# Optimization experiments

Measured on AMD Instinct MI355X. Metric: run time of the kernel, lower is better.

Reference implementation:

```python
import jax, jax.numpy as jnp
import numpy as np

B, C, H, W, NH = 4, 96, 256, 256, 4


def setup_inputs() -> dict:
    key = jax.random.key(0)
    ks = jax.random.split(key, 8)
    s = 0.05  # keep pre-activations well-scaled
    return {
        "x": jax.random.normal(ks[0], (B, C, H, W), jnp.float32),
        "ff": jax.random.normal(ks[1], (B, C, H, W), jnp.float32),
        "w_q": jax.random.normal(ks[2], (C, C, 1, 1), jnp.float32) * s,
        "w_kv": jax.random.normal(ks[3], (2 * C, C, 1, 1), jnp.float32) * s,
        "w_q_dw": jax.random.normal(ks[4], (C, 1, 3, 3), jnp.float32) * s,
        "w_kv_dw": jax.random.normal(ks[5], (2 * C, 1, 3, 3), jnp.float32) * s,
        "w_out": jax.random.normal(ks[6], (C, C, 1, 1), jnp.float32) * s,
        "temperature": jnp.ones((NH, 1, 1), jnp.float32),
    }


def _conv1x1(x, w):
    # pointwise conv == channel GEMM; w: [O, I, 1, 1]
    return jnp.einsum('bchw,oc->bohw', x, w[:, :, 0, 0])


def _dwconv3(x, w):
    # depthwise 3x3, padding=1; w: [C, 1, 3, 3]
    return jax.lax.conv_general_dilated(
        x, w, window_strides=(1, 1), padding='SAME',
        feature_group_count=x.shape[1],
        dimension_numbers=('NCHW', 'OIHW', 'NCHW'))


def _l2norm(t, eps=1e-12):
    # L2-normalize along last (HW) axis, torch F.normalize semantics
    n = jnp.sqrt(jnp.sum(t * t, axis=-1, keepdims=True))
    return t / jnp.maximum(n, eps)


def reference(x, ff, w_q, w_kv, w_q_dw, w_kv_dw, w_out, temperature):
    b, c, h, w = x.shape
    q = _dwconv3(_conv1x1(ff, w_q), w_q_dw)          # [B,C,H,W]
    kv = _dwconv3(_conv1x1(x, w_kv), w_kv_dw)        # [B,2C,H,W]
    k, v = jnp.split(kv, 2, axis=1)

    def heads(t):
        return t.reshape(b, NH, c // NH, h * w)       # [B,nh,c,HW]

    q = _l2norm(heads(q))
    k = _l2norm(heads(k))
    v = heads(v)
    # channel-wise (transposed) attention: [B,nh,c,c]
    attn = jax.nn.softmax(jnp.einsum('bhcn,bhdn->bhcd', q, k) * temperature, axis=-1)
    o = jnp.einsum('bhcd,bhdn->bhcn', attn, v).reshape(b, c, h, w)
    return _conv1x1(o, w_out)
```

## Files before the change

### kernel.cpp

```cpp
#include <hip/hip_runtime.h>
#include <hip/hip_bf16.h>
#include <hip/hip_fp16.h>

typedef unsigned int u32;
typedef unsigned short u16;
typedef unsigned char u8;
typedef _Float16 f16;

static constexpr int HWn = 65536;

typedef __attribute__((ext_vector_type(8))) f16 f16x8;
typedef __attribute__((ext_vector_type(2))) f16 f16x2;
typedef __attribute__((ext_vector_type(4))) float f32x4;
typedef __attribute__((ext_vector_type(2))) float f32x2;

__device__ __forceinline__ float h2f(u16 u) {
    union { u16 s; f16 h; } z; z.s = u; return (float)z.h;
}
__device__ __forceinline__ u16 f2h(float f) {
    union { u16 s; f16 h; } z; z.h = (f16)f; return z.s;
}
__device__ __forceinline__ u32 pack2h(float a, float b) {
    union { u32 i; f16 h[2]; } z; z.h[0] = (f16)a; z.h[1] = (f16)b; return z.i;
}
__device__ __forceinline__ float hlo(u32 u) {
    union { u32 i; f16 h[2]; } z; z.i = u; return (float)z.h[0];
}
__device__ __forceinline__ float hhi(u32 u) {
    union { u32 i; f16 h[2]; } z; z.i = u; return (float)z.h[1];
}
__device__ __forceinline__ float sq2h(u32 a) {
    const float l = hlo(a), h = hhi(a);
    return fmaf(l, l, h * h);
}

#if defined(__has_builtin)
#if __has_builtin(__builtin_amdgcn_fdot2)
#define HAS_FDOT2 1
#endif
#endif
__device__ __forceinline__ float fdot2a(u32 a, u32 b, float c) {
#ifdef HAS_FDOT2
    union { u32 i; f16x2 h; } A, B; A.i = a; B.i = b;
    return __builtin_amdgcn_fdot2(A.h, B.h, c, false);
#else
    return fmaf(hlo(a), hlo(b), fmaf(hhi(a), hhi(b), c));
#endif
}

__device__ __forceinline__ int xoff(int px, int icb) {
    return px * 128 + (((icb ^ (px & 7) ^ ((px >> 3) & 7))) << 3);
}

__global__ __launch_bounds__(256) void k_prep_w(
    const float* __restrict__ wq, const float* __restrict__ wkv,
    u16* __restrict__ wf)
{
    const int i = blockIdx.x * 256 + threadIdx.x;
    if (i >= 288 * 96) return;
    const int row = i / 96, ic = i % 96;
    const float w = (row < 96) ? wq[row * 96 + ic] : wkv[(row - 96) * 96 + ic];
    wf[i] = f2h(w);
}

__global__ __launch_bounds__(256, 3) void k_conv_mfma(
    const float* __restrict__ ff, const float* __restrict__ x,
    const u16* __restrict__ wf,
    u8* __restrict__ qk8, u16* __restrict__ v16)
{
    const int b = blockIdx.z, sec = blockIdx.y;
    const int pxb = blockIdx.x * 256;
    const int tid = threadIdx.x;

    __shared__ __align__(16) u16 xs[16384];

    const float* src = (sec == 0 ? ff : x) + (size_t)b * 96 * HWn;
    const int icq = (tid >> 4) * 2;
    const int pxs = (tid & 15) * 8;
    const int lane = tid & 63;
    const int wv = tid >> 6;
    const int oc0 = (wv >> 1) * 48;
    const int pxw = (wv & 1) * 64;
    const int lr = lane & 15, lg = lane >> 4;

    float4 L[12];

    auto issue = [&](int x0) {
        #pragma unroll
        for (int p = 0; p < 3; ++p) {
            const float* rp0 = src + (size_t)(p * 32 + icq) * HWn + x0 + pxs;
            const float* rp1 = rp0 + HWn;
            L[p * 4 + 0] = *reinterpret_cast<const float4*>(rp0);
            L[p * 4 + 1] = *reinterpret_cast<const float4*>(rp0 + 4);
            L[p * 4 + 2] = *reinterpret_cast<const float4*>(rp1);
            L[p * 4 + 3] = *reinterpret_cast<const float4*>(rp1 + 4);
        }
    };
    auto stage = [&]() {
        #pragma unroll
        for (int p = 0; p < 3; ++p) {
            const int ic = p * 32 + icq;
            const int icb = ic >> 3, icl = ic & 7;
            const float e0[8] = {L[p*4+0].x, L[p*4+0].y, L[p*4+0].z, L[p*4+0].w,
                                 L[p*4+1].x, L[p*4+1].y, L[p*4+1].z, L[p*4+1].w};
            const float e1[8] = {L[p*4+2].x, L[p*4+2].y, L[p*4+2].z, L[p*4+2].w,
                                 L[p*4+3].x, L[p*4+3].y, L[p*4+3].z, L[p*4+3].w};
            #pragma unroll
            for (int j = 0; j < 8; ++j) {
                const int o = xoff(pxs + j, icb) + icl;
                *reinterpret_cast<u32*>(&xs[o]) = pack2h(e0[j], e1[j]);
            }
        }
    };
    auto compute = [&](int x0) {
        const int npass = (sec == 0) ? 1 : 2;
        #pragma unroll 1
        for (int kvs = 0; kvs < npass; ++kvs) {
            const u16* wh = wf + ((sec == 0) ? 0 : (96 + kvs * 96)) * 96;
            const bool isv = (sec == 1) && (kvs == 1);
            f32x4 acc[4][3];
            #pragma unroll
            for (int n = 0; n < 4; ++n)
                #pragma unroll
                for (int m = 0; m < 3; ++m)
                    acc[n][m] = (f32x4){0.f, 0.f, 0.f, 0.f};

            #pragma unroll 1
            for (int kt = 0; kt < 3; ++kt) {
                const int kb = kt * 32;
                f16x8 XA[4];
                #pragma unroll
                for (int n = 0; n < 4; ++n)
                    XA[n] = *(const f16x8*)(xs + xoff(pxw + n * 16 + lr, (kb >> 3) + lg));
                f16x8 WB[3];
                #pragma unroll
                for (int m = 0; m < 3; ++m)
                    WB[m] = *(const f16x8*)(wh + (oc0 + m * 16 + lr) * 96 + kb + lg * 8);
                #pragma unroll
                for (int n = 0; n < 4; ++n)
                    #pragma unroll
                    for (int m = 0; m < 3; ++m)
                        acc[n][m] = __builtin_amdgcn_mfma_f32_16x16x32_f16(XA[n], WB[m], acc[n][m], 0, 0, 0);
            }

            if (!isv) {
                u8* dst8 = qk8 + ((size_t)b * 192 + (sec == 0 ? 0 : 96)) * (size_t)HWn;
                #pragma unroll
                for (int n = 0; n < 4; ++n) {
                    #pragma unroll
                    for (int m = 0; m < 3; ++m) {
                        const int oc = oc0 + m * 16 + lr;
                        u32 pk = (u32)__builtin_amdgcn_cvt_pk_fp8_f32(acc[n][m][0], acc[n][m][1], 0, false);
                        pk = (u32)__builtin_amdgcn_cvt_pk_fp8_f32(acc[n][m][2], acc[n][m][3], (int)pk, true);
                        *reinterpret_cast<u32*>(dst8 + (size_t)oc * HWn + x0 + pxw + n * 16 + lg * 4) = pk;
                    }
                }
            } else {
                u16* dstv = v16 + (size_t)b * 96 * HWn;
                #pragma unroll
                for (int n = 0; n < 4; ++n) {
                    #pragma unroll
                    for (int m = 0; m < 3; ++m) {
                        const int oc = oc0 + m * 16 + lr;
                        ushort4 sv;
                        sv.x = f2h(acc[n][m][0]); sv.y = f2h(acc[n][m][1]);
                        sv.z = f2h(acc[n][m][2]); sv.w = f2h(acc[n][m][3]);
                        *reinterpret_cast<ushort4*>(dstv + (size_t)oc * HWn + x0 + pxw + n * 16 + lg * 4) = sv;
                    }
                }
            }
        }
    };

    issue(pxb);
    stage();
    __syncthreads();
    issue(pxb + 128);
    compute(pxb);
    __syncthreads();
    stage();
    __syncthreads();
    compute(pxb + 128);
}

__device__ __forceinline__ void row3tap(
    const uint4 m, u32 lv, u32 rv, u32 w01, u32 w2z, float* a)
{
    const u32 P0 = m.x, P1 = m.y, P2 = m.z, P3 = m.w;
    const u32 s0 = (lv >> 16) | (P0 << 16);
    const u32 s1 = (P0 >> 16) | (P1 << 16);
    const u32 s2 = (P1 >> 16) | (P2 << 16);
    const u32 s3 = (P2 >> 16) | (P3 << 16);
    const u32 s4 = (P3 >> 16) | (rv << 16);
    a[0] = fdot2a(w2z, s1, fdot2a(w01, s0, a[0]));
    a[1] = fdot2a(w2z, P1, fdot2a(w01, P0, a[1]));
    a[2] = fdot2a(w2z, s2, fdot2a(w01, s1, a[2]));
    a[3] = fdot2a(w2z, P2, fdot2a(w01, P1, a[3]));
    a[4] = fdot2a(w2z, s3, fdot2a(w01, s2, a[4]));
    a[5] = fdot2a(w2z, P3, fdot2a(w01, P2, a[5]));
    a[6] = fdot2a(w2z, s4, fdot2a(w01, s3, a[6]));
    a[7] = fdot2a(w2z, rv, fdot2a(w01, P3, a[7]));
}

__global__ __launch_bounds__(512) void k_dw_qk(
    const u8* __restrict__ qk8,
    const float* __restrict__ wqdw, const float* __restrict__ wkvdw,
    float* __restrict__ ssq, float* __restrict__ Sg)
{
    const int bid = blockIdx.x;
    const int wg = (bid & 7) * 256 + (bid >> 3);
    const int b = wg >> 9;
    const int rem = wg & 511;
    const int y = rem >> 1;
    const int tx = (rem & 1) * 128;
    const int tid = threadIdx.x;
    const int lane = tid & 63;
    const int pq = tid >> 4;
    const int chunk = tid & 15;
    const int x0l = chunk * 8;
    const int xg = tx + x0l;

    const bool vr0 = (y > 0), vr2 = (y < 255);
    const bool le = (chunk == 0) && (xg > 0);
    const bool re = (chunk == 15) && (xg + 8 < 256);

    __shared__ __align__(16) u16 qs[96][136];
    __shared__ __align__(16) u16 ks[96][136];

    auto addr = [&](int it, const u8*& r0, const float*& wp, int& c, int& seg) {
        const int p = it * 32 + pq;
        r0 = qk8 + ((size_t)(b * 192 + p)) * HWn + (y - 1) * 256 + xg;
        if (p < 96) { c = p;      wp = wqdw  + p * 9;        seg = 0; }
        else        { c = p - 96; wp = wkvdw + (p - 96) * 9; seg = 1; }
    };
    auto issue = [&](const u8* r0, uint2* m, u32* el, u32* er) {
        const uint2 z = make_uint2(0u, 0u);
        const u8* r1 = r0 + 256;
        const u8* r2 = r1 + 256;
        m[0] = vr0 ? *reinterpret_cast<const uint2*>(r0) : z;
        m[1] = *reinterpret_cast<const uint2*>(r1);
        m[2] = vr2 ? *reinterpret_cast<const uint2*>(r2) : z;
        el[0] = (le && vr0) ? ((u32)r0[-1] << 24) : 0u;  er[0] = (re && vr0) ? (u32)r0[8] : 0u;
        el[1] = le ? ((u32)r1[-1] << 24) : 0u;           er[1] = re ? (u32)r1[8] : 0u;
        el[2] = (le && vr2) ? ((u32)r2[-1] << 24) : 0u;  er[2] = (re && vr2) ? (u32)r2[8] : 0u;
    };

    const u8* srcC; const float* wpC; int cC, segC;
    addr(0, srcC, wpC, cC, segC);
    uint2 mcur[3]; u32 elc[3], erc[3];
    issue(srcC, mcur, elc, erc);

    #pragma unroll 1
    for (int it = 0; it < 6; ++it) {
        const u8* srcN; const float* wpN; int cN, segN;
        uint2 mnx[3]; u32 eln[3], ern[3];
        if (it < 5) {
            addr(it + 1, srcN, wpN, cN, segN);
            issue(srcN, mnx, eln, ern);
        }

        float a[8] = {0.f, 0.f, 0.f, 0.f, 0.f, 0.f, 0.f, 0.f};
        #pragma unroll
        for (int r = 0; r < 3; ++r) {
            const uint2 u = mcur[r];
            const f32x2 p01 = __builtin_amdgcn_cvt_pk_f32_fp8((int)u.x, false);
            const f32x2 p23 = __builtin_amdgcn_cvt_pk_f32_fp8((int)u.x, true);
            const f32x2 p45 = __builtin_amdgcn_cvt_pk_f32_fp8((int)u.y, false);
            const f32x2 p67 = __builtin_amdgcn_cvt_pk_f32_fp8((int)u.y, true);
            const u32 ln = (u32)__shfl((int)u.y, (lane - 1) & 63);
            const u32 rn = (u32)__shfl((int)u.x, (lane + 1) & 63);
            const u32 lsel = (chunk == 0)  ? elc[r] : ln;
            const u32 rsel = (chunk == 15) ? erc[r] : rn;
            const f32x2 lcv = __builtin_amdgcn_cvt_pk_f32_fp8((int)lsel, true);
            const f32x2 rcv = __builtin_amdgcn_cvt_pk_f32_fp8((int)rsel, false);
            const float v[10] = {
                lcv[1],
                p01[0], p01[1], p23[0], p23[1], p45[0], p45[1], p67[0], p67[1],
                rcv[0]
            };
            const float w0 = wpC[r * 3 + 0], w1 = wpC[r * 3 + 1], w2 = wpC[r * 3 + 2];
            #pragma unroll
            for (int j = 0; j < 8; ++j)
                a[j] = fmaf(w0, v[j], fmaf(w1, v[j + 1], fmaf(w2, v[j + 2], a[j])));
        }

        const uint4 o = make_uint4(pack2h(a[0], a[1]), pack2h(a[2], a[3]),
                                   pack2h(a[4], a[5]), pack2h(a[6], a[7]));
        if (segC == 0) *reinterpret_cast<uint4*>(&qs[cC][x0l]) = o;
        else           *reinterpret_cast<uint4*>(&ks[cC][x0l]) = o;

        if (it < 5) {
            #pragma unroll
            for (int r = 0; r < 3; ++r) { mcur[r] = mnx[r]; elc[r] = eln[r]; erc[r] = ern[r]; }
            wpC = wpN; cC = cN; segC = segN;
        }
    }
    __syncthreads();

    if (tid < 384) {
        const int half = tid >= 192;
        const int r = tid - half * 192;
        const uint4* rr = reinterpret_cast<const uint4*>(
            (r < 96 ? &qs[r][0] : &ks[r - 96][0]) + half * 64);
        float s = 0.f;
        #pragma unroll
        for (int pch = 0; pch < 8; ++pch) {
            const uint4 a = rr[pch];
            s += sq2h(a.x) + sq2h(a.y) + sq2h(a.z) + sq2h(a.w);
        }
        atomicAdd(ssq + b * 192 + r, s);
    }

    {
        const int w = tid >> 6;
        const int h = w & 3, mt = w >> 2;
        const int lr2 = lane & 15, lg2 = lane >> 4;
        const int ar = h * 24 + min(mt * 16 + lr2, 23);
        f32x4 acc2[2];
        acc2[0] = (f32x4){0.f, 0.f, 0.f, 0.f};
        acc2[1] = (f32x4){0.f, 0.f, 0.f, 0.f};
        #pragma unroll
        for (int ks4 = 0; ks4 < 4; ++ks4) {
            const f16x8 A = *(const f16x8*)(&qs[ar][ks4 * 32 + lg2 * 8]);
            #pragma unroll
            for (int nt = 0; nt < 2; ++nt) {
                const int bc = h * 24 + min(nt * 16 + lr2, 23);
                const f16x8 B = *(const f16x8*)(&ks[bc][ks4 * 32 + lg2 * 8]);
                acc2[nt] = __builtin_amdgcn_mfma_f32_16x16x32_f16(A, B, acc2[nt], 0, 0, 0);
            }
        }
        #pragma unroll
        for (int nt = 0; nt < 2; ++nt) {
            const int col = nt * 16 + lr2;
            #pragma unroll
            for (int reg = 0; reg < 4; ++reg) {
                const int row24 = mt * 16 + lg2 * 4 + reg;
                if (row24 < 24 && col < 24)
                    atomicAdd(Sg + b * 2304 + h * 576 + row24 * 24 + col, acc2[nt][reg]);
            }
        }
    }
}

__global__ __launch_bounds__(256) void k_attn_fold(
    const float* __restrict__ ssq, const float* __restrict__ S,
    const float* __restrict__ temp, const float* __restrict__ w_out,
    u16* __restrict__ mf)
{
    const int b = blockIdx.x;
    const int tid = threadIdx.x;
    __shared__ float rq[96], rk[96], att[2304];

    if (tid < 96) {
        rq[tid] = 1.f / fmaxf(sqrtf(ssq[b * 192 + tid]), 1e-12f);
    } else if (tid < 192) {
        const int c = tid - 96;
        rk[c] = 1.f / fmaxf(sqrtf(ssq[b * 192 + 96 + c]), 1e-12f);
    }
    __syncthreads();

    if (tid < 96) {
        const int h = tid / 24, i = tid % 24;
        const float tmp = temp[h];
        const float rqi = rq[h * 24 + i];
        float l[24];
        float m = -1e30f;
        #pragma unroll
        for (int j = 0; j < 24; ++j) {
            l[j] = S[b * 2304 + (h * 24 + i) * 24 + j] * rqi * rk[h * 24 + j] * tmp;
            m = fmaxf(m, l[j]);
        }
        float ssum = 0.f;
        #pragma unroll
        for (int j = 0; j < 24; ++j) { l[j] = expf(l[j] - m); ssum += l[j]; }
        const float inv = 1.f / ssum;
        #pragma unroll
        for (int j = 0; j < 24; ++j) att[(h * 24 + i) * 24 + j] = l[j] * inv;
    }
    __syncthreads();

    for (int k = 0; k < 36; ++k) {
        const int id = k * 256 + tid;
        const int dg = id / 96, oc = id % 96;
        const int h = dg / 24, d24 = dg % 24;
        float s = 0.f;
        #pragma unroll
        for (int i = 0; i < 24; ++i) {
            s += w_out[oc * 96 + h * 24 + i] * att[(h * 24 + i) * 24 + d24];
        }
        mf[b * 9216 + oc * 96 + dg] = f2h(s);
    }
}

__global__ __launch_bounds__(256, 4) void k_v_out(
    const u16* __restrict__ v16, const float* __restrict__ wkvdw,
    const u16* __restrict__ mf, float* __restrict__ out)
{
    const int bid = blockIdx.x;
    const int wg = (bid & 7) * 256 + (bid >> 3);
    const int b = wg >> 9;
    const int rem = wg & 511;
    const int y = rem >> 1;
    const int tx = (rem & 1) * 128;
    const int tid = threadIdx.x;
    const int lane = tid & 63;
    const int slot = tid >> 4;
    const int chunk = tid & 15;
    const int x0l = chunk * 8;
    const int xg = tx + x0l;

    const bool vr0 = (y > 0), vr2 = (y < 255);
    const bool le = (chunk == 0) && (xg > 0);
    const bool re = (chunk == 15) && (xg + 8 < 256);

    __shared__ __align__(16) u16 xt[16384];

    auto issue = [&](int it, uint4* m0, uint4* m1, u32* e0l, u32* e0r, u32* e1l, u32* e1r) {
        const int dg = (it * 16 + slot) * 2;
        const u16* s0 = v16 + ((size_t)(b * 96 + dg)) * HWn + (y - 1) * 256 + xg;
        const u16* s1 = s0 + HWn;
        const uint4 z = make_uint4(0u, 0u, 0u, 0u);
        m0[0] = vr0 ? *reinterpret_cast<const uint4*>(s0)       : z;
        m0[1] =       *reinterpret_cast<const uint4*>(s0 + 256);
        m0[2] = vr2 ? *reinterpret_cast<const uint4*>(s0 + 512) : z;
        m1[0] = vr0 ? *reinterpret_cast<const uint4*>(s1)       : z;
        m1[1] =       *reinterpret_cast<const uint4*>(s1 + 256);
        m1[2] = vr2 ? *reinterpret_cast<const uint4*>(s1 + 512) : z;
        e0l[0] = (le && vr0) ? ((u32)s0[-1] << 16) : 0u;   e0r[0] = (re && vr0) ? (u32)s0[8] : 0u;
        e0l[1] = le ? ((u32)s0[255] << 16) : 0u;           e0r[1] = re ? (u32)s0[264] : 0u;
        e0l[2] = (le && vr2) ? ((u32)s0[511] << 16) : 0u;  e0r[2] = (re && vr2) ? (u32)s0[520] : 0u;
        e1l[0] = (le && vr0) ? ((u32)s1[-1] << 16) : 0u;   e1r[0] = (re && vr0) ? (u32)s1[8] : 0u;
        e1l[1] = le ? ((u32)s1[255] << 16) : 0u;           e1r[1] = re ? (u32)s1[264] : 0u;
        e1l[2] = (le && vr2) ? ((u32)s1[511] << 16) : 0u;  e1r[2] = (re && vr2) ? (u32)s1[520] : 0u;
    };

    uint4 m0c[3], m1c[3]; u32 e0lc[3], e0rc[3], e1lc[3], e1rc[3];
    issue(0, m0c, m1c, e0lc, e0rc, e1lc, e1rc);

    #pragma unroll 1
    for (int it = 0; it < 3; ++it) {
        uint4 m0n[3], m1n[3]; u32 e0ln[3], e0rn[3], e1ln[3], e1rn[3];
        if (it < 2) issue(it + 1, m0n, m1n, e0ln, e0rn, e1ln, e1rn);

        const int dg = (it * 16 + slot) * 2;
        const float* wp0 = wkvdw + (96 + dg) * 9;
        const float* wp1 = wp0 + 9;

        float a0[8] = {0.f, 0.f, 0.f, 0.f, 0.f, 0.f, 0.f, 0.f};
        float a1[8] = {0.f, 0.f, 0.f, 0.f, 0.f, 0.f, 0.f, 0.f};
        #pragma unroll
        for (int r = 0; r < 3; ++r) {
            {
                const u32 w01 = pack2h(wp0[r * 3 + 0], wp0[r * 3 + 1]);
                const u32 w2z = pack2h(wp0[r * 3 + 2], 0.f);
                const u32 lvn = __shfl((int)m0c[r].w, (lane - 1) & 63);
                const u32 rvn = __shfl((int)m0c[r].x, (lane + 1) & 63);
                const u32 lv = (chunk == 0)  ? e0lc[r] : lvn;
                const u32 rv = (chunk == 15) ? e0rc[r] : rvn;
                row3tap(m0c[r], lv, rv, w01, w2z, a0);
            }
            {
                const u32 w01 = pack2h(wp1[r * 3 + 0], wp1[r * 3 + 1]);
                const u32 w2z = pack2h(wp1[r * 3 + 2], 0.f);
                const u32 lvn = __shfl((int)m1c[r].w, (lane - 1) & 63);
                const u32 rvn = __shfl((int)m1c[r].x, (lane + 1) & 63);
                const u32 lv = (chunk == 0)  ? e1lc[r] : lvn;
                const u32 rv = (chunk == 15) ? e1rc[r] : rvn;
                row3tap(m1c[r], lv, rv, w01, w2z, a1);
            }
        }

        const int icb = dg >> 3, icl = dg & 7;
        #pragma unroll
        for (int j = 0; j < 8; ++j) {
            *reinterpret_cast<u32*>(&xt[xoff(x0l + j, icb) + icl]) = pack2h(a0[j], a1[j]);
        }

        if (it < 2) {
            #pragma unroll
            for (int r = 0; r < 3; ++r) {
                m0c[r] = m0n[r]; m1c[r] = m1n[r];
                e0lc[r] = e0ln[r]; e0rc[r] = e0rn[r];
                e1lc[r] = e1ln[r]; e1rc[r] = e1rn[r];
            }
        }
    }
    __syncthreads();

    const u16* mh = mf + b * 9216;
    const int wv = tid >> 6;
    const int oc0 = (wv >> 1) * 48;
    const int pxw = (wv & 1) * 64;
    const int lr = lane & 15, lg = lane >> 4;

    f32x4 acc[4][3];
    #pragma unroll
    for (int n = 0; n < 4; ++n)
        #pragma unroll
        for (int m = 0; m < 3; ++m)
            acc[n][m] = (f32x4){0.f, 0.f, 0.f, 0.f};

    #pragma unroll 1
    for (int kt = 0; kt < 3; ++kt) {
        const int kb = kt * 32;
        f16x8 XA[4];
        #pragma unroll
        for (int n = 0; n < 4; ++n)
            XA[n] = *(const f16x8*)(xt + xoff(pxw + n * 16 + lr, (kb >> 3) + lg));
        f16x8 WB[3];
        #pragma unroll
        for (int m = 0; m < 3; ++m)
            WB[m] = *(const f16x8*)(mh + (oc0 + m * 16 + lr) * 96 + kb + lg * 8);
        #pragma unroll
        for (int n = 0; n < 4; ++n)
            #pragma unroll
            for (int m = 0; m < 3; ++m)
                acc[n][m] = __builtin_amdgcn_mfma_f32_16x16x32_f16(XA[n], WB[m], acc[n][m], 0, 0, 0);
    }

    #pragma unroll
    for (int n = 0; n < 4; ++n) {
        #pragma unroll
        for (int m = 0; m < 3; ++m) {
            const int oc = oc0 + m * 16 + lr;
            float* drow = out + ((size_t)(b * 96 + oc)) * HWn + y * 256 + tx;
            const float4 o4 = make_float4(acc[n][m][0], acc[n][m][1], acc[n][m][2], acc[n][m][3]);
            *reinterpret_cast<float4*>(drow + pxw + n * 16 + lg * 4) = o4;
        }
    }
}

extern "C" void kernel_launch(void* const* d_in, const int* in_sizes, int n_in,
                              void* d_out, int out_size, void* d_ws, size_t ws_size,
                              hipStream_t stream) {
    (void)in_sizes; (void)n_in; (void)out_size; (void)ws_size;
    const float* x      = (const float*)d_in[0];
    const float* ff     = (const float*)d_in[1];
    const float* w_q    = (const float*)d_in[2];
    const float* w_kv   = (const float*)d_in[3];
    const float* w_q_dw = (const float*)d_in[4];
    const float* w_kv_dw= (const float*)d_in[5];
    const float* w_out  = (const float*)d_in[6];
    const float* temp   = (const float*)d_in[7];
    float* out = (float*)d_out;

    char* ws = (char*)d_ws;
    u8* qk8     = (u8*)(ws);
    u16* v16    = (u16*)(ws + 50331648);
    float* ssq  = (float*)(ws + 100663296);
    float* S    = (float*)(ws + 100666368);
    u16* wf     = (u16*)(ws + 100703232);
    u16* mf     = (u16*)(ws + 100758528);

    hipMemsetAsync(ws + 100663296, 0, 3072 + 36864, stream);

    k_prep_w<<<108, 256, 0, stream>>>(w_q, w_kv, wf);
    k_conv_mfma<<<dim3(256, 2, 4), 256, 0, stream>>>(ff, x, wf, qk8, v16);
    k_dw_qk<<<dim3(2048), 512, 0, stream>>>(qk8, w_q_dw, w_kv_dw, ssq, S);
    k_attn_fold<<<4, 256, 0, stream>>>(ssq, S, temp, w_out, mf);
    k_v_out<<<dim3(2048), 256, 0, stream>>>(v16, w_kv_dw, mf, out);
}
```

Before: 248.8 us.

## Double-buffer LDS and register loads in pointwise conv, four tiles per block

The 1x1 conv kernel now handles four 128-pixel tiles per block instead of two. It ping-pongs two LDS buffers and two register staging arrays, so the global load of the next tile is issued while the current tile's MFMAs run. Each tile step needs one barrier instead of two. In exchange the block holds twice the LDS and register staging, the occupancy hint drops from 3 to 2 blocks per CU, and the grid is halved.

```diff
diff --git a/kernel.cpp b/kernel.cpp
--- a/kernel.cpp
+++ b/kernel.cpp
@@ -63,16 +63,16 @@
     wf[i] = f2h(w);
 }
 
-__global__ __launch_bounds__(256, 3) void k_conv_mfma(
+__global__ __launch_bounds__(256, 2) void k_conv_mfma(
     const float* __restrict__ ff, const float* __restrict__ x,
     const u16* __restrict__ wf,
     u8* __restrict__ qk8, u16* __restrict__ v16)
 {
     const int b = blockIdx.z, sec = blockIdx.y;
-    const int pxb = blockIdx.x * 256;
+    const int pxg = blockIdx.x * 512;
     const int tid = threadIdx.x;
 
-    __shared__ __align__(16) u16 xs[16384];
+    __shared__ __align__(16) u16 xs[2][16384];
 
     const float* src = (sec == 0 ? ff : x) + (size_t)b * 96 * HWn;
     const int icq = (tid >> 4) * 2;
@@ -83,12 +83,12 @@
     const int pxw = (wv & 1) * 64;
     const int lr = lane & 15, lg = lane >> 4;
 
-    float4 L[12];
-
-    auto issue = [&](int x0) {
+    float4 L0[12], L1[12];
+
+    auto issue = [&](int px0, float4* L) {
         #pragma unroll
         for (int p = 0; p < 3; ++p) {
-            const float* rp0 = src + (size_t)(p * 32 + icq) * HWn + x0 + pxs;
+            const float* rp0 = src + (size_t)(p * 32 + icq) * HWn + px0 + pxs;
             const float* rp1 = rp0 + HWn;
             L[p * 4 + 0] = *reinterpret_cast<const float4*>(rp0);
             L[p * 4 + 1] = *reinterpret_cast<const float4*>(rp0 + 4);
@@ -96,7 +96,7 @@
             L[p * 4 + 3] = *reinterpret_cast<const float4*>(rp1 + 4);
         }
     };
-    auto stage = [&]() {
+    auto stage = [&](const float4* L, u16* xsb) {
         #pragma unroll
         for (int p = 0; p < 3; ++p) {
             const int ic = p * 32 + icq;
@@ -108,11 +108,11 @@
             #pragma unroll
             for (int j = 0; j < 8; ++j) {
                 const int o = xoff(pxs + j, icb) + icl;
-                *reinterpret_cast<u32*>(&xs[o]) = pack2h(e0[j], e1[j]);
+                *reinterpret_cast<u32*>(&xsb[o]) = pack2h(e0[j], e1[j]);
             }
         }
     };
-    auto compute = [&](int x0) {
+    auto compute = [&](const u16* xsb, int x0) {
         const int npass = (sec == 0) ? 1 : 2;
         #pragma unroll 1
         for (int kvs = 0; kvs < npass; ++kvs) {
@@ -131,7 +131,7 @@
                 f16x8 XA[4];
                 #pragma unroll
                 for (int n = 0; n < 4; ++n)
-                    XA[n] = *(const f16x8*)(xs + xoff(pxw + n * 16 + lr, (kb >> 3) + lg));
+                    XA[n] = *(const f16x8*)(xsb + xoff(pxw + n * 16 + lr, (kb >> 3) + lg));
                 f16x8 WB[3];
                 #pragma unroll
                 for (int m = 0; m < 3; ++m)
@@ -172,15 +172,22 @@
         }
     };
 
-    issue(pxb);
-    stage();
-    __syncthreads();
-    issue(pxb + 128);
-    compute(pxb);
-    __syncthreads();
-    stage();
-    __syncthreads();
-    compute(pxb + 128);
+    issue(pxg, L0);
+    stage(L0, xs[0]);
+    issue(pxg + 128, L1);
+    __syncthreads();
+    compute(xs[0], pxg);
+    stage(L1, xs[1]);
+    issue(pxg + 256, L0);
+    __syncthreads();
+    compute(xs[1], pxg + 128);
+    stage(L0, xs[0]);
+    issue(pxg + 384, L1);
+    __syncthreads();
+    compute(xs[0], pxg + 256);
+    stage(L1, xs[1]);
+    __syncthreads();
+    compute(xs[1], pxg + 384);
 }
 
 __device__ __forceinline__ void row3tap(
@@ -555,7 +562,7 @@
     hipMemsetAsync(ws + 100663296, 0, 3072 + 36864, stream);
 
     k_prep_w<<<108, 256, 0, stream>>>(w_q, w_kv, wf);
-    k_conv_mfma<<<dim3(256, 2, 4), 256, 0, stream>>>(ff, x, wf, qk8, v16);
+    k_conv_mfma<<<dim3(128, 2, 4), 256, 0, stream>>>(ff, x, wf, qk8, v16);
     k_dw_qk<<<dim3(2048), 512, 0, stream>>>(qk8, w_q_dw, w_kv_dw, ssq, S);
     k_attn_fold<<<4, 256, 0, stream>>>(ssq, S, temp, w_out, mf);
     k_v_out<<<dim3(2048), 256, 0, stream>>>(v16, w_kv_dw, mf, out);
```

Result: no change. 249.5 us (+0.3%).
